# Kernel tuning notes

Hardware: AMD Instinct MI355X
Metric: run time of the kernel (lower is better)

The kernel has to match this reference:

```python
import jax, jax.numpy as jnp
import numpy as np

# Module / grid constants (match init_kwargs and chosen input scale)
B, H, W = 2, 512, 512
SIZE, NIN, NOUT = 3, 64, 64
STRIDE, INV_STRIDE = 1, 1
N_NZ = 131072   # active input cells
N_MASK = 131072 # active output (mask) cells


def setup_inputs() -> dict:
    key = jax.random.key(0)
    ks = jax.random.split(key, 10)
    values = jax.random.normal(ks[0], (N_NZ, NIN), dtype=jnp.float32)
    # init matches torch: uniform in [-stdv, stdv]
    stdv = 1.0 / np.sqrt(float(SIZE * SIZE * NIN))
    kernel = (jax.random.uniform(ks[1], (SIZE, SIZE, NIN, NOUT), dtype=jnp.float32) - 0.5) * 2.0 * stdv
    bias = (jax.random.uniform(ks[2], (NOUT,), dtype=jnp.float32) - 0.5) * 2.0 * stdv
    ib = jax.random.randint(ks[3], (N_NZ,), 0, B)
    iy = jax.random.randint(ks[4], (N_NZ,), 0, H)
    ix = jax.random.randint(ks[5], (N_NZ,), 0, W)
    indices = jnp.stack([ib, iy, ix], axis=1).astype(jnp.int64)  # [N,3] like input.indices().T
    mb = jax.random.randint(ks[6], (N_MASK,), 0, B)
    my = jax.random.randint(ks[7], (N_MASK,), 0, H * INV_STRIDE // STRIDE)
    mx = jax.random.randint(ks[8], (N_MASK,), 0, W * INV_STRIDE // STRIDE)
    mask_indices = jnp.stack([mb, my, mx], axis=1).astype(jnp.int64)
    mask_values = jnp.ones((N_MASK, 1), dtype=jnp.float32)
    return {"values": values, "kernel": kernel, "bias": bias,
            "mask_values": mask_values, "indices": indices, "mask_indices": mask_indices}


def reference(values, kernel, bias, mask_values, indices, mask_indices):
    # Sparse octree conv: per kernel tap, gather-matmul-scatter with index
    # shift/scale and clamping to the output grid (clamped taps pile up on
    # the border exactly as torch.maximum/minimum do in the original).
    Ho = H // STRIDE * INV_STRIDE
    Wo = W // STRIDE * INV_STRIDE
    half = SIZE // 2
    b = indices[:, 0]
    dense = jnp.zeros((B, Ho, Wo, NOUT), dtype=values.dtype)
    for ky in range(SIZE):
        for kx in range(SIZE):
            v = values @ kernel[ky, kx]  # [N, nout]
            sy = jnp.clip((indices[:, 1] * INV_STRIDE + (ky - half)) // STRIDE, 0, Ho - 1)
            sx = jnp.clip((indices[:, 2] * INV_STRIDE + (kx - half)) // STRIDE, 0, Wo - 1)
            dense = dense.at[b, sy, sx].add(v)  # scatter-add == coalesce-sum
    # densified mask (duplicates sum, matching COO coalesce semantics)
    mask = jnp.zeros((B, Ho, Wo, 1), dtype=values.dtype)
    mask = mask.at[mask_indices[:, 0], mask_indices[:, 1], mask_indices[:, 2]].add(mask_values)
    # result = (result + mask * bias) * mask  (with_bias=True, mask nonempty)
    out = (dense + mask * bias) * mask
    return out
```

## Files before the change

### kernel.cpp

```cpp
#include <hip/hip_runtime.h>

#define BATCH 2
#define HH 512
#define WW 512
#define NIN 64
#define NOUT 64
#define N_NZ 131072
#define N_MASK 131072
#define NPIX (BATCH * HH * WW)
#define PPW 64
#define MAX_ALIVE N_MASK

#define WS_MASK_OFF   256
#define WS_CMP_OFF    (WS_MASK_OFF + (size_t)NPIX * 4)
#define WS_SLOT_OFF   (WS_CMP_OFF + (size_t)MAX_ALIVE * NOUT * 4)
#define WS_NEED       (WS_SLOT_OFF + (size_t)NPIX * 4)
#define WS_MEMSET     WS_CMP_OFF

__global__ void mask_scatter_kernel(const float* __restrict__ mv,
                                    const int* __restrict__ midx,
                                    float* __restrict__ mask) {
    int n = blockIdx.x * blockDim.x + threadIdx.x;
    if (n < N_MASK) {
        int b = midx[n * 3 + 0];
        int y = midx[n * 3 + 1];
        int x = midx[n * 3 + 2];
        atomicAdd(&mask[(b * HH + y) * WW + x], mv[n]);
    }
}

__global__ __launch_bounds__(256) void build_slot3_kernel(
        const float* __restrict__ mask,
        int* __restrict__ slot,
        int* __restrict__ counter,
        float4* __restrict__ compactz) {
    const int ztot = MAX_ALIVE * NOUT / 4;
    const float4 z4 = make_float4(0.f, 0.f, 0.f, 0.f);
    for (int z = blockIdx.x * 256 + threadIdx.x; z < ztot; z += 512 * 256)
        compactz[z] = z4;

    const int tid = threadIdx.x;
    const int gid = blockIdx.x * 256 + tid;
    const float4 m = reinterpret_cast<const float4*>(mask)[gid];
    const int c0 = (m.x != 0.f) + (m.y != 0.f) + (m.z != 0.f) + (m.w != 0.f);

    const int lane = tid & 63;
    const int wv = tid >> 6;
    int pre = c0;
#pragma unroll
    for (int d = 1; d < 64; d <<= 1) {
        int t = __shfl_up(pre, d);
        if (lane >= d) pre += t;
    }

    __shared__ int wsum[4];
    __shared__ int wbase[4];
    __shared__ int blockbase;
    if (lane == 63) wsum[wv] = pre;
    __syncthreads();
    if (tid == 0) {
        int s = 0;
#pragma unroll
        for (int w = 0; w < 4; ++w) { wbase[w] = s; s += wsum[w]; }
        blockbase = atomicAdd(counter, s);
    }
    __syncthreads();

    int s0 = blockbase + wbase[wv] + (pre - c0);
    int4 sv;
    sv.x = (m.x != 0.f) ? s0++ : -1;
    sv.y = (m.y != 0.f) ? s0++ : -1;
    sv.z = (m.z != 0.f) ? s0++ : -1;
    sv.w = (m.w != 0.f) ? s0++ : -1;
    reinterpret_cast<int4*>(slot)[gid] = sv;
}

__global__ __launch_bounds__(256, 2) void conv_scatter6_kernel(
        const float* __restrict__ values,
        const float* __restrict__ kern,
        const int* __restrict__ idx,
        const int* __restrict__ slot,
        float* __restrict__ compact) {
    const int wv   = threadIdx.x >> 6;
    const int wg   = blockIdx.x * 4 + wv;
    const int tap  = wg % 9;
    const int tile = wg / 9;
    const int lane = threadIdx.x & 63;
    const int ky = tap / 3;
    const int kx = tap % 3;

    __shared__ __align__(16) float rows[4][2][4][NIN];

    float kreg[NIN];
    const float* kp = kern + (size_t)tap * NIN * NOUT + lane;
#pragma unroll
    for (int i = 0; i < NIN; ++i) kreg[i] = kp[(size_t)i * NOUT];
#pragma unroll
    for (int i = 0; i < NIN; ++i) asm volatile("" : "+v"(kreg[i]));

    const int p0 = tile * PPW;
    const int p  = p0 + lane;
    const int b = idx[p * 3 + 0];
    const int y = idx[p * 3 + 1];
    const int x = idx[p * 3 + 2];
    const int sy = min(max(y + ky - 1, 0), HH - 1);
    const int sx = min(max(x + kx - 1, 0), WW - 1);
    const int pix = (b * HH + sy) * WW + sx;
    const int s = slot[pix];

    unsigned long long mrem = __ballot(s >= 0);
    int cnt = __popcll(mrem);

    int J0 = 0, J1 = 0, J2 = 0, J3 = 0;
    float c0 = 0.f, c1 = 0.f, c2 = 0.f, c3 = 0.f;
    if (cnt >= 4) {
        J0 = __ffsll((long long)mrem) - 1; mrem &= mrem - 1;
        J1 = __ffsll((long long)mrem) - 1; mrem &= mrem - 1;
        J2 = __ffsll((long long)mrem) - 1; mrem &= mrem - 1;
        J3 = __ffsll((long long)mrem) - 1; mrem &= mrem - 1;
        c0 = values[(size_t)(p0 + J0) * NIN + lane];
        c1 = values[(size_t)(p0 + J1) * NIN + lane];
        c2 = values[(size_t)(p0 + J2) * NIN + lane];
        c3 = values[(size_t)(p0 + J3) * NIN + lane];
    }
    int pc = 0;
    while (cnt >= 4) {
        cnt -= 4;
        const int s0 = __shfl(s, J0);
        const int s1 = __shfl(s, J1);
        const int s2 = __shfl(s, J2);
        const int s3 = __shfl(s, J3);
        float* rw = &rows[wv][pc][0][0];
        rw[0 * NIN + lane] = c0;
        rw[1 * NIN + lane] = c1;
        rw[2 * NIN + lane] = c2;
        rw[3 * NIN + lane] = c3;
        float n0 = 0.f, n1 = 0.f, n2 = 0.f, n3 = 0.f;
        if (cnt >= 4) {
            J0 = __ffsll((long long)mrem) - 1; mrem &= mrem - 1;
            J1 = __ffsll((long long)mrem) - 1; mrem &= mrem - 1;
            J2 = __ffsll((long long)mrem) - 1; mrem &= mrem - 1;
            J3 = __ffsll((long long)mrem) - 1; mrem &= mrem - 1;
            n0 = values[(size_t)(p0 + J0) * NIN + lane];
            n1 = values[(size_t)(p0 + J1) * NIN + lane];
            n2 = values[(size_t)(p0 + J2) * NIN + lane];
            n3 = values[(size_t)(p0 + J3) * NIN + lane];
        }
        const float4* q0 = reinterpret_cast<const float4*>(rw + 0 * NIN);
        const float4* q1 = reinterpret_cast<const float4*>(rw + 1 * NIN);
        const float4* q2 = reinterpret_cast<const float4*>(rw + 2 * NIN);
        const float4* q3 = reinterpret_cast<const float4*>(rw + 3 * NIN);
        float a0 = 0.f, a1 = 0.f, a2 = 0.f, a3 = 0.f;
#pragma unroll
        for (int i4 = 0; i4 < 16; ++i4) {
            const float4 w0 = q0[i4];
            const float4 w1 = q1[i4];
            const float4 w2 = q2[i4];
            const float4 w3 = q3[i4];
            a0 = fmaf(w0.x, kreg[4 * i4 + 0], a0);
            a0 = fmaf(w0.y, kreg[4 * i4 + 1], a0);
            a0 = fmaf(w0.z, kreg[4 * i4 + 2], a0);
            a0 = fmaf(w0.w, kreg[4 * i4 + 3], a0);
            a1 = fmaf(w1.x, kreg[4 * i4 + 0], a1);
            a1 = fmaf(w1.y, kreg[4 * i4 + 1], a1);
            a1 = fmaf(w1.z, kreg[4 * i4 + 2], a1);
            a1 = fmaf(w1.w, kreg[4 * i4 + 3], a1);
            a2 = fmaf(w2.x, kreg[4 * i4 + 0], a2);
            a2 = fmaf(w2.y, kreg[4 * i4 + 1], a2);
            a2 = fmaf(w2.z, kreg[4 * i4 + 2], a2);
            a2 = fmaf(w2.w, kreg[4 * i4 + 3], a2);
            a3 = fmaf(w3.x, kreg[4 * i4 + 0], a3);
            a3 = fmaf(w3.y, kreg[4 * i4 + 1], a3);
            a3 = fmaf(w3.z, kreg[4 * i4 + 2], a3);
            a3 = fmaf(w3.w, kreg[4 * i4 + 3], a3);
        }
        atomicAdd(&compact[(size_t)s0 * NOUT + lane], a0);
        atomicAdd(&compact[(size_t)s1 * NOUT + lane], a1);
        atomicAdd(&compact[(size_t)s2 * NOUT + lane], a2);
        atomicAdd(&compact[(size_t)s3 * NOUT + lane], a3);
        c0 = n0; c1 = n1; c2 = n2; c3 = n3;
        pc ^= 1;
    }
    while (mrem) {
        const int j = __ffsll((long long)mrem) - 1; mrem &= mrem - 1;
        const int sj = __shfl(s, j);
        const float* vp = values + (size_t)(p0 + j) * NIN;
        float a = 0.f;
#pragma unroll
        for (int i = 0; i < NIN; ++i) a = fmaf(vp[i], kreg[i], a);
        atomicAdd(&compact[(size_t)sj * NOUT + lane], a);
    }
}

__global__ void finalize2_kernel(float* __restrict__ out,
                                 const float* __restrict__ mask,
                                 const int* __restrict__ slot,
                                 const float* __restrict__ compact,
                                 const float* __restrict__ bias) {
    const int t = blockIdx.x * blockDim.x + threadIdx.x;
    const int p = t >> 4;
    const int c4 = (t & 15) * 4;
    if (p >= NPIX) return;
    float4* o = reinterpret_cast<float4*>(out + (size_t)p * NOUT + c4);
    const int s = slot[p];
    if (s < 0) {
        *o = make_float4(0.f, 0.f, 0.f, 0.f);
        return;
    }
    const float m = mask[p];
    const float4 bb = *reinterpret_cast<const float4*>(bias + c4);
    float4 v = *reinterpret_cast<const float4*>(compact + (size_t)s * NOUT + c4);
    v.x = (v.x + m * bb.x) * m;
    v.y = (v.y + m * bb.y) * m;
    v.z = (v.z + m * bb.z) * m;
    v.w = (v.w + m * bb.w) * m;
    *o = v;
}

__global__ __launch_bounds__(64, 2) void conv_scatter_kernel(
        const float* __restrict__ values,
        const float* __restrict__ kern,
        const int* __restrict__ idx,
        const float* __restrict__ mask,
        float* __restrict__ dense) {
    const int bid  = blockIdx.x;
    const int tap  = bid % 9;
    const int tile = bid / 9;
    const int lane = threadIdx.x;
    const int ky = tap / 3;
    const int kx = tap % 3;
    float kreg[NIN];
    const float* kp = kern + (size_t)tap * NIN * NOUT + lane;
#pragma unroll
    for (int i = 0; i < NIN; ++i) kreg[i] = kp[(size_t)i * NOUT];
#pragma unroll
    for (int i = 0; i < NIN; ++i) asm volatile("" : "+v"(kreg[i]));
    const int p0 = tile * PPW;
    for (int pp = 0; pp < PPW; ++pp) {
        const int p = p0 + pp;
        const int b = idx[p * 3 + 0];
        const int y = idx[p * 3 + 1];
        const int x = idx[p * 3 + 2];
        const int sy = min(max(y + ky - 1, 0), HH - 1);
        const int sx = min(max(x + kx - 1, 0), WW - 1);
        const size_t pix = ((size_t)b * HH + sy) * WW + sx;
        if (mask[pix] != 0.0f) {
            const float* vp = values + (size_t)p * NIN;
            float acc = 0.0f;
#pragma unroll
            for (int i = 0; i < NIN; ++i) acc = fmaf(vp[i], kreg[i], acc);
            atomicAdd(&dense[pix * NOUT + lane], acc);
        }
    }
}

__global__ void finalize_kernel(float* __restrict__ out,
                                const float* __restrict__ mask,
                                const float* __restrict__ bias) {
    const int t = blockIdx.x * blockDim.x + threadIdx.x;
    const int p = t >> 4;
    const int c4 = (t & 15) * 4;
    if (p >= NPIX) return;
    const float m = mask[p];
    if (m == 0.0f) return;
    float4* o = reinterpret_cast<float4*>(out + (size_t)p * NOUT + c4);
    const float4 bb = *reinterpret_cast<const float4*>(bias + c4);
    float4 v = *o;
    v.x = (v.x + m * bb.x) * m;
    v.y = (v.y + m * bb.y) * m;
    v.z = (v.z + m * bb.z) * m;
    v.w = (v.w + m * bb.w) * m;
    *o = v;
}

extern "C" void kernel_launch(void* const* d_in, const int* in_sizes, int n_in,
                              void* d_out, int out_size, void* d_ws, size_t ws_size,
                              hipStream_t stream) {
    const float* values      = (const float*)d_in[0];
    const float* kern        = (const float*)d_in[1];
    const float* bias        = (const float*)d_in[2];
    const float* mask_values = (const float*)d_in[3];
    const int*   indices     = (const int*)d_in[4];
    const int*   mask_idx    = (const int*)d_in[5];
    float* out = (float*)d_out;

    if (ws_size >= WS_NEED) {
        char* ws = (char*)d_ws;
        int*   counter = (int*)ws;
        float* mask    = (float*)(ws + WS_MASK_OFF);
        float* compact = (float*)(ws + WS_CMP_OFF);
        int*   slot    = (int*)(ws + WS_SLOT_OFF);

        hipMemsetAsync(ws, 0, WS_MEMSET, stream);

        mask_scatter_kernel<<<(N_MASK + 255) / 256, 256, 0, stream>>>(
            mask_values, mask_idx, mask);
        build_slot3_kernel<<<NPIX / 4 / 256, 256, 0, stream>>>(
            mask, slot, counter, (float4*)compact);

        const int nwaves = 9 * (N_NZ / PPW);
        conv_scatter6_kernel<<<nwaves / 4, 256, 0, stream>>>(
            values, kern, indices, slot, compact);

        const int total = NPIX * (NOUT / 4);
        finalize2_kernel<<<(total + 255) / 256, 256, 0, stream>>>(
            out, mask, slot, compact, bias);
    } else {
        float* mask = (float*)d_ws;
        hipMemsetAsync(out, 0, (size_t)out_size * sizeof(float), stream);
        hipMemsetAsync(mask, 0, (size_t)NPIX * sizeof(float), stream);
        mask_scatter_kernel<<<(N_MASK + 255) / 256, 256, 0, stream>>>(
            mask_values, mask_idx, mask);
        const int nblocks = 9 * (N_NZ / PPW);
        conv_scatter_kernel<<<nblocks, 64, 0, stream>>>(
            values, kern, indices, mask, out);
        const int total = NPIX * (NOUT / 4);
        finalize_kernel<<<(total + 255) / 256, 256, 0, stream>>>(out, mask, bias);
    }
}
```

Before: 250.7 us.

## Fuse memset, mask scatter and slot build into one cooperative kernel

Replaces the workspace memset, the mask scatter kernel and the slot-building kernel with a single cooperative kernel that uses grid-wide syncs between the zeroing, atomic mask scatter and prefix-scan phases. The goal is to remove two launch boundaries and a separate memset pass. It requires all 512 blocks to be co-resident for cooperative launch, and grid.sync has its own cost. The zeroing of the compact buffer is also restructured into a fixed strided loop.

```diff
diff --git a/kernel.cpp b/kernel.cpp
--- a/kernel.cpp
+++ b/kernel.cpp
@@ -1,4 +1,7 @@
 #include <hip/hip_runtime.h>
+#include <hip/hip_cooperative_groups.h>
+
+namespace cg = cooperative_groups;
 
 #define BATCH 2
 #define HH 512
@@ -15,42 +18,44 @@
 #define WS_CMP_OFF    (WS_MASK_OFF + (size_t)NPIX * 4)
 #define WS_SLOT_OFF   (WS_CMP_OFF + (size_t)MAX_ALIVE * NOUT * 4)
 #define WS_NEED       (WS_SLOT_OFF + (size_t)NPIX * 4)
-#define WS_MEMSET     WS_CMP_OFF
-
-__global__ void mask_scatter_kernel(const float* __restrict__ mv,
-                                    const int* __restrict__ midx,
-                                    float* __restrict__ mask) {
-    int n = blockIdx.x * blockDim.x + threadIdx.x;
-    if (n < N_MASK) {
-        int b = midx[n * 3 + 0];
-        int y = midx[n * 3 + 1];
-        int x = midx[n * 3 + 2];
-        atomicAdd(&mask[(b * HH + y) * WW + x], mv[n]);
-    }
-}
-
-__global__ __launch_bounds__(256) void build_slot3_kernel(
-        const float* __restrict__ mask,
+
+__global__ __launch_bounds__(256) void front_kernel(
+        const float* __restrict__ mv,
+        const int* __restrict__ midx,
+        float* __restrict__ mask,
         int* __restrict__ slot,
         int* __restrict__ counter,
         float4* __restrict__ compactz) {
-    const int ztot = MAX_ALIVE * NOUT / 4;
+    cg::grid_group grid = cg::this_grid();
+    const int tid = blockIdx.x * 256 + threadIdx.x;
+
     const float4 z4 = make_float4(0.f, 0.f, 0.f, 0.f);
-    for (int z = blockIdx.x * 256 + threadIdx.x; z < ztot; z += 512 * 256)
-        compactz[z] = z4;
-
-    const int tid = threadIdx.x;
-    const int gid = blockIdx.x * 256 + tid;
-    const float4 m = reinterpret_cast<const float4*>(mask)[gid];
+    reinterpret_cast<float4*>(mask)[tid] = z4;
+#pragma unroll
+    for (int k = 0; k < 16; ++k)
+        compactz[(size_t)k * (N_MASK) + tid] = z4;
+    if (tid == 0) *counter = 0;
+    grid.sync();
+
+    {
+        const int b = midx[tid * 3 + 0];
+        const int y = midx[tid * 3 + 1];
+        const int x = midx[tid * 3 + 2];
+        atomicAdd(&mask[(b * HH + y) * WW + x], mv[tid]);
+    }
+    grid.sync();
+
+    const int t = threadIdx.x;
+    const float4 m = reinterpret_cast<const float4*>(mask)[tid];
     const int c0 = (m.x != 0.f) + (m.y != 0.f) + (m.z != 0.f) + (m.w != 0.f);
 
-    const int lane = tid & 63;
-    const int wv = tid >> 6;
+    const int lane = t & 63;
+    const int wv = t >> 6;
     int pre = c0;
 #pragma unroll
     for (int d = 1; d < 64; d <<= 1) {
-        int t = __shfl_up(pre, d);
-        if (lane >= d) pre += t;
+        int tt = __shfl_up(pre, d);
+        if (lane >= d) pre += tt;
     }
 
     __shared__ int wsum[4];
@@ -58,7 +63,7 @@
     __shared__ int blockbase;
     if (lane == 63) wsum[wv] = pre;
     __syncthreads();
-    if (tid == 0) {
+    if (t == 0) {
         int s = 0;
 #pragma unroll
         for (int w = 0; w < 4; ++w) { wbase[w] = s; s += wsum[w]; }
@@ -72,7 +77,7 @@
     sv.y = (m.y != 0.f) ? s0++ : -1;
     sv.z = (m.z != 0.f) ? s0++ : -1;
     sv.w = (m.w != 0.f) ? s0++ : -1;
-    reinterpret_cast<int4*>(slot)[gid] = sv;
+    reinterpret_cast<int4*>(slot)[tid] = sv;
 }
 
 __global__ __launch_bounds__(256, 2) void conv_scatter6_kernel(
@@ -217,6 +222,18 @@
     *o = v;
 }
 
+__global__ void mask_scatter_kernel(const float* __restrict__ mv,
+                                    const int* __restrict__ midx,
+                                    float* __restrict__ mask) {
+    int n = blockIdx.x * blockDim.x + threadIdx.x;
+    if (n < N_MASK) {
+        int b = midx[n * 3 + 0];
+        int y = midx[n * 3 + 1];
+        int x = midx[n * 3 + 2];
+        atomicAdd(&mask[(b * HH + y) * WW + x], mv[n]);
+    }
+}
+
 __global__ __launch_bounds__(64, 2) void conv_scatter_kernel(
         const float* __restrict__ values,
         const float* __restrict__ kern,
@@ -291,12 +308,12 @@
         float* compact = (float*)(ws + WS_CMP_OFF);
         int*   slot    = (int*)(ws + WS_SLOT_OFF);
 
-        hipMemsetAsync(ws, 0, WS_MEMSET, stream);
-
-        mask_scatter_kernel<<<(N_MASK + 255) / 256, 256, 0, stream>>>(
-            mask_values, mask_idx, mask);
-        build_slot3_kernel<<<NPIX / 4 / 256, 256, 0, stream>>>(
-            mask, slot, counter, (float4*)compact);
+        float4* compact4 = (float4*)compact;
+        void* fargs[] = {(void*)&mask_values, (void*)&mask_idx, (void*)&mask,
+                         (void*)&slot, (void*)&counter, (void*)&compact4};
+        hipLaunchCooperativeKernel((const void*)front_kernel,
+                                   dim3(NPIX / 4 / 256), dim3(256),
+                                   fargs, 0, stream);
 
         const int nwaves = 9 * (N_NZ / PPW);
         conv_scatter6_kernel<<<nwaves / 4, 256, 0, stream>>>(
```

Result: slower. 374.4 us (+49.4%).
